# Kernel optimization log

Measured on AMD Instinct MI355X. Metric: run time of the kernel, lower is better.

Reference implementation:

```python
import jax, jax.numpy as jnp
import numpy as np

B, C, D, L, CTX = 8, 320, 24, 77, 768
NUM_GROUPS = 32
EPS = 1e-5


def setup_inputs() -> dict:
    key = jax.random.key(0)
    ks = jax.random.split(key, 8)
    s = 0.02
    return {
        "x": jax.random.normal(ks[0], (B, C, D, D, D), jnp.float32),
        "context": jax.random.normal(ks[1], (B, L, CTX), jnp.float32),
        "Wq": jax.random.normal(ks[2], (C, C), jnp.float32) * s,
        "bq": jnp.zeros((C,), jnp.float32),
        "Wk": jax.random.normal(ks[3], (C, CTX), jnp.float32) * s,
        "bk": jnp.zeros((C,), jnp.float32),
        "Wv": jax.random.normal(ks[4], (C, CTX), jnp.float32) * s,
        "bv": jnp.zeros((C,), jnp.float32),
        "Wo": jax.random.normal(ks[5], (C, C), jnp.float32) * s,
        "bo": jnp.zeros((C,), jnp.float32),
        "gamma": jnp.ones((C,), jnp.float32),
        "beta": jnp.zeros((C,), jnp.float32),
    }


def reference(x, context, Wq, bq, Wk, bk, Wv, bv, Wo, bo, gamma, beta):
    b, c = x.shape[:2]
    spatial = x.shape[2:]
    xf = x.reshape(b, c, -1)                                # [B, C, N]
    # 1x1 Conv3d == per-position channel matmul
    q = jnp.einsum('oc,bcn->bon', Wq, xf) + bq[None, :, None]
    ctx_t = context.transpose(0, 2, 1)                      # [B, CTX, L]
    k = jnp.einsum('oc,bcl->bol', Wk, ctx_t) + bk[None, :, None]
    v = jnp.einsum('oc,bcl->bol', Wv, ctx_t) + bv[None, :, None]
    # scores [B, N, L], scaled by C^-0.5 (int(C) in the original)
    qk = jnp.einsum('bcn,bcl->bnl', q, k) * (float(c) ** -0.5)
    w = jax.nn.softmax(qk, axis=-1)
    h = jnp.einsum('bcl,bnl->bcn', v, w)                    # [B, C, N]
    h = jnp.einsum('oc,bcn->bon', Wo, h) + bo[None, :, None]
    xr = h + xf                                             # residual
    # GroupNorm over (C/G, spatial) per group
    g = NUM_GROUPS
    xg = xr.reshape(b, g, -1)
    mu = jnp.mean(xg, axis=-1, keepdims=True)
    var = jnp.var(xg, axis=-1, keepdims=True)
    xn = ((xg - mu) * jax.lax.rsqrt(var + EPS)).reshape(b, c, -1)
    xn = xn * gamma[None, :, None] + beta[None, :, None]
    out = xn * jax.nn.sigmoid(xn)                           # Swish
    return out.reshape(b, c, *spatial)
```

## Files before the change

kernel.cpp:

```cpp
#include <hip/hip_runtime.h>
#include <hip/hip_bf16.h>

#define B_ 8
#define C_ 320
#define N_ 13824
#define L_ 77
#define LP 80
#define LV 96
#define CTXD 768
#define CPG 10
#define EPS_ 1e-5f
#define SCALE_ 0.05590169943749474f

typedef __attribute__((__ext_vector_type__(4))) float f32x4;
typedef __attribute__((__ext_vector_type__(8))) short s16x8;

#define WS_ACCUM 0
#define WS_T     2048
#define WS_KST   4608
#define WS_VST   414208
#define WS_K2F   823808
#define WS_V2F   1233408
#define WS_WQT   1724928
#define WS_WO    1929728
#define WS_WGF   2134528

__device__ __forceinline__ unsigned short f2bf(float f) {
  union { float f; unsigned u; } v; v.f = f;
  unsigned r = v.u + 0x7FFFu + ((v.u >> 16) & 1u);
  return (unsigned short)(r >> 16);
}
__device__ __forceinline__ float bf2f(unsigned short s) {
  union { unsigned u; float f; } v; v.u = ((unsigned)s) << 16;
  return v.f;
}
__device__ __forceinline__ s16x8 cvt8(const float* p) {
  f32x4 a = *reinterpret_cast<const f32x4*>(p);
  f32x4 b = *reinterpret_cast<const f32x4*>(p + 4);
  s16x8 r;
  r[0] = (short)f2bf(a[0]); r[1] = (short)f2bf(a[1]);
  r[2] = (short)f2bf(a[2]); r[3] = (short)f2bf(a[3]);
  r[4] = (short)f2bf(b[0]); r[5] = (short)f2bf(b[1]);
  r[6] = (short)f2bf(b[2]); r[7] = (short)f2bf(b[3]);
  return r;
}
__device__ __forceinline__ f32x4 MFMA(s16x8 a, s16x8 b, f32x4 c) {
  return __builtin_amdgcn_mfma_f32_16x16x32_bf16(a, b, c, 0, 0, 0);
}

__global__ __launch_bounds__(256) void prep_kernel(const float* __restrict__ Wq,
                                                   const float* __restrict__ Wo,
                                                   const float* __restrict__ ctx,
                                                   const float* __restrict__ Wk,
                                                   const float* __restrict__ bk,
                                                   const float* __restrict__ Wv,
                                                   const float* __restrict__ bv,
                                                   unsigned short* __restrict__ wqT,
                                                   unsigned short* __restrict__ wo_bf,
                                                   unsigned short* __restrict__ kst,
                                                   unsigned short* __restrict__ vst,
                                                   float* __restrict__ zws) {
  int bid = blockIdx.x;
  if (bid < 400) {
    int t = bid * 256 + threadIdx.x;
    if (t >= C_ * C_) return;
    int o = t / C_, c = t - o * C_;
    wqT[c * C_ + o] = f2bf(Wq[t]);
    wo_bf[t] = f2bf(Wo[t]);
    return;
  }
  int kb = bid - 400;
  { int t = kb * 256 + threadIdx.x; if (t < 1152) zws[t] = 0.f; }
  int lt = kb % 5;
  int kb5 = kb / 5;
  int b = kb5 / 5;
  int oc = kb5 % 5;
  int w = threadIdx.x >> 6, lane = threadIdx.x & 63;
  int r = lane & 15, h = lane >> 4;
  int o_row = oc * 64 + w * 16 + r;
  int l = lt * 16 + r;
  bool lok = (l < L_);
  f32x4 ak = {}, av = {};
  for (int ks = 0; ks < 24; ++ks) {
    int c0 = ks * 32 + h * 8;
    s16x8 aWk = cvt8(Wk + o_row * CTXD + c0);
    s16x8 aWv = cvt8(Wv + o_row * CTXD + c0);
    s16x8 bfr = {0,0,0,0,0,0,0,0};
    if (lok) bfr = cvt8(ctx + (b * L_ + l) * CTXD + c0);
    ak = MFMA(aWk, bfr, ak);
    av = MFMA(aWv, bfr, av);
  }
#pragma unroll
  for (int j = 0; j < 4; ++j) {
    int o = oc * 64 + w * 16 + h * 4 + j;
    float bkv = bk[o], bvv = bv[o];
    unsigned short kw = lok ? f2bf(SCALE_ * (ak[j] + bkv)) : (unsigned short)0;
    unsigned short vw = lok ? f2bf(av[j] + bvv) : (unsigned short)0;
    kst[(b * LP + l) * C_ + o] = kw;
    vst[(b * LP + l) * C_ + o] = vw;
  }
}

__global__ __launch_bounds__(256) void kv2_kernel(const unsigned short* __restrict__ wqT,
                                                  const unsigned short* __restrict__ wo_bf,
                                                  const unsigned short* __restrict__ kst,
                                                  const unsigned short* __restrict__ vst,
                                                  const float* __restrict__ bq,
                                                  float* __restrict__ tbuf,
                                                  unsigned short* __restrict__ k2F,
                                                  unsigned short* __restrict__ v2F) {
  int b = blockIdx.x / 5;
  int cc = blockIdx.x % 5;
  int w = threadIdx.x >> 6, lane = threadIdx.x & 63;
  int r = lane & 15, h = lane >> 4;
  int c_row = cc * 64 + w * 16 + r;
  f32x4 a2[5] = {}, av[5] = {};
#pragma unroll
  for (int ks = 0; ks < 10; ++ks) {
    int o0 = ks * 32 + h * 8;
    s16x8 aq = *reinterpret_cast<const s16x8*>(wqT + c_row * C_ + o0);
    s16x8 ao = *reinterpret_cast<const s16x8*>(wo_bf + c_row * C_ + o0);
#pragma unroll
    for (int nt = 0; nt < 5; ++nt) {
      int l = nt * 16 + r;
      s16x8 bk_ = *reinterpret_cast<const s16x8*>(kst + (b * LP + l) * C_ + o0);
      s16x8 bv_ = *reinterpret_cast<const s16x8*>(vst + (b * LP + l) * C_ + o0);
      a2[nt] = MFMA(aq, bk_, a2[nt]);
      av[nt] = MFMA(ao, bv_, av[nt]);
    }
  }
#pragma unroll
  for (int j = 0; j < 4; ++j) {
    int c = cc * 64 + w * 16 + h * 4 + j;
    int ks2 = c >> 5, h2 = (c >> 3) & 3, j2 = c & 7;
    int cs = c / 80, mt = (c - cs * 80) >> 4, rc = c & 15;
#pragma unroll
    for (int nt = 0; nt < 5; ++nt) {
      int l = nt * 16 + r;
      k2F[(((b * 5 + nt) * 10 + ks2) << 9) + ((h2 * 16 + r) << 3) + j2] = f2bf(a2[nt][j]);
      int ksl = l >> 5, hl = (l >> 3) & 3, jl = l & 7;
      v2F[((((long)(b * 4 + cs) * 5 + mt) * 3 + ksl) << 9) + ((hl * 16 + rc) << 3) + jl]
          = f2bf(av[nt][j]);
    }
  }
  {
    int t = threadIdx.x;
    int m = cc * 4 + (t >> 6);
    int cs = m / 5, mt = m % 5;
    long base = (((long)(b * 4 + cs) * 5 + mt) * 3 + 2) << 9;
    *reinterpret_cast<unsigned long long*>(v2F + base + 256 + (t & 63) * 4) = 0ull;
  }
  if (cc == 0 && threadIdx.x < LP) {
    int l = threadIdx.x;
    float acc = 0.f;
    for (int o8 = 0; o8 < C_; o8 += 8) {
      s16x8 kv = *reinterpret_cast<const s16x8*>(kst + (b * LP + l) * C_ + o8);
#pragma unroll
      for (int j = 0; j < 8; ++j) acc += bq[o8 + j] * bf2f((unsigned short)kv[j]);
    }
    tbuf[b * LP + l] = acc;
  }
}

__global__ __launch_bounds__(256)
__attribute__((amdgpu_waves_per_eu(2, 3)))
void fusedS_kernel(const float* __restrict__ x,
                   const unsigned short* __restrict__ k2F,
                   const float* __restrict__ tbuf,
                   unsigned short* __restrict__ wglF) {
  __shared__ __align__(16) unsigned short tile[64][344];
  char* tb = (char*)&tile[0][0];
  int bid = blockIdx.x;
  int b = bid & 7;
  int tileIdx = bid >> 3;
  int n0 = tileIdx * 64;
  int tid = threadIdx.x;
  int w = tid >> 6, lane = tid & 63, r = lane & 15, h = lane >> 4;
  const unsigned short* k2f = k2F + ((long)b * 50 << 9);

  s16x8 kfA[5], kfB[5];
#pragma unroll
  for (int nt = 0; nt < 5; ++nt)
    kfA[nt] = *reinterpret_cast<const s16x8*>(k2f + ((nt * 10) << 9) + (lane << 3));

  {
    int s_ = tid & 15;
    int cp = tid >> 4;
    const float* xb = x + (long)b * C_ * N_ + n0 + s_ * 4;
    f32x4 va[10], vb[10];
#pragma unroll
    for (int it = 0; it < 10; ++it) {
      const float* p = xb + (long)(it * 32 + cp * 2) * N_;
      va[it] = *reinterpret_cast<const f32x4*>(p);
      vb[it] = *reinterpret_cast<const f32x4*>(p + N_);
    }
#pragma unroll
    for (int it = 0; it < 10; ++it) {
      int cbyte = (it * 32 + cp * 2) * 2;
#pragma unroll
      for (int q = 0; q < 4; ++q) {
        int row = s_ * 4 + q;
        unsigned pk = (unsigned)f2bf(va[it][q]) | ((unsigned)f2bf(vb[it][q]) << 16);
        *reinterpret_cast<unsigned*>(tb + row * 688 + (cbyte ^ (row & 48))) = pk;
      }
    }
  }
  __syncthreads();

  int arow = w * 16 + r;
  int abase = arow * 688;
  int akey = arow & 48;
  f32x4 sacc[5] = {};
#define SCHUNK(KS, KC, KN)                                                      \
  {                                                                             \
    s16x8 a = *reinterpret_cast<const s16x8*>(                                  \
        tb + abase + (((KS * 32 + h * 8) * 2) ^ akey));                         \
    if (KS < 9) {                                                               \
      _Pragma("unroll") for (int nt = 0; nt < 5; ++nt)                          \
          KN[nt] = *reinterpret_cast<const s16x8*>(                             \
              k2f + ((nt * 10 + KS + 1) << 9) + (lane << 3));                   \
    }                                                                           \
    _Pragma("unroll") for (int nt = 0; nt < 5; ++nt)                            \
      sacc[nt] = MFMA(a, KC[nt], sacc[nt]);                                     \
  }
  SCHUNK(0, kfA, kfB) SCHUNK(1, kfB, kfA) SCHUNK(2, kfA, kfB)
  SCHUNK(3, kfB, kfA) SCHUNK(4, kfA, kfB) SCHUNK(5, kfB, kfA)
  SCHUNK(6, kfA, kfB) SCHUNK(7, kfB, kfA) SCHUNK(8, kfA, kfB)
  SCHUNK(9, kfB, kfA)
#undef SCHUNK

#pragma unroll
  for (int nt = 0; nt < 5; ++nt) {
    float tl = tbuf[b * LP + nt * 16 + r];
#pragma unroll
    for (int j = 0; j < 4; ++j) sacc[nt][j] += tl;
  }
  long wbase = ((long)(b * 216 + tileIdx) * 12) << 9;
  bool maskpad = (r >= 13);
#pragma unroll
  for (int j = 0; j < 4; ++j) {
    float m = -1e30f;
#pragma unroll
    for (int nt = 0; nt < 5; ++nt) {
      float v = (nt == 4 && maskpad) ? -1e30f : sacc[nt][j];
      m = fmaxf(m, v);
    }
    for (int d = 1; d < 16; d <<= 1) m = fmaxf(m, __shfl_xor(m, d));
    float e[5]; float sum = 0.f;
#pragma unroll
    for (int nt = 0; nt < 5; ++nt) {
      float v = (nt == 4 && maskpad) ? 0.f : __expf(sacc[nt][j] - m);
      e[nt] = v; sum += v;
    }
    for (int d = 1; d < 16; d <<= 1) sum += __shfl_xor(sum, d);
    float inv = 1.f / sum;
    int r2 = h * 4 + j;
#pragma unroll
    for (int nt = 0; nt < 5; ++nt) {
      int l = nt * 16 + r;
      int ks = l >> 5, h2 = (l >> 3) & 3, j2 = l & 7;
      wglF[wbase + ((ks * 4 + w) << 9) + ((h2 * 16 + r2) << 3) + j2] = f2bf(e[nt] * inv);
    }
  }
  {
    int t = tid;
    *reinterpret_cast<unsigned long long*>(
        wglF + wbase + ((2 * 4 + (t >> 6)) << 9) + 256 + (t & 63) * 4) = 0ull;
  }
}

__global__ __launch_bounds__(256)
__attribute__((amdgpu_waves_per_eu(2, 3)))
void mainH_kernel(const float* __restrict__ x,
                  const unsigned short* __restrict__ wglF,
                  const unsigned short* __restrict__ v2F,
                  const float* __restrict__ bo,
                  float* __restrict__ accum,
                  float* __restrict__ hout) {
  __shared__ float ch[C_][2];
  int bid = blockIdx.x;
  int b = bid & 7;
  int tileIdx = bid >> 3;
  int n0 = tileIdx * 64;
  int tid = threadIdx.x;
  int w = tid >> 6, lane = tid & 63, r = lane & 15, h = lane >> 4;
  const unsigned short* wf = wglF + (((long)(b * 216 + tileIdx) * 12) << 9);
  const unsigned short* vf = v2F + (((long)(b * 4 + w) * 15) << 9);
  const float* xb = x + (long)b * C_ * N_ + n0;

  f32x4 acc[4][5] = {};
#pragma unroll
  for (int ks = 0; ks < 3; ++ks) {
    s16x8 bf[4];
#pragma unroll
    for (int nt = 0; nt < 4; ++nt)
      bf[nt] = *reinterpret_cast<const s16x8*>(wf + ((ks * 4 + nt) << 9) + (lane << 3));
#pragma unroll
    for (int mt = 0; mt < 5; ++mt) {
      s16x8 va = *reinterpret_cast<const s16x8*>(vf + ((mt * 3 + ks) << 9) + (lane << 3));
#pragma unroll
      for (int nt = 0; nt < 4; ++nt) acc[nt][mt] = MFMA(va, bf[nt], acc[nt][mt]);
    }
  }
#pragma unroll
  for (int mt = 0; mt < 5; ++mt) {
    int cb = w * 80 + mt * 16 + h * 4;
    float bov[4];
#pragma unroll
    for (int j = 0; j < 4; ++j) bov[j] = bo[cb + j];
    float sv[4] = {0.f, 0.f, 0.f, 0.f}, sq[4] = {0.f, 0.f, 0.f, 0.f};
#pragma unroll
    for (int nt = 0; nt < 4; ++nt) {
      int n = nt * 16 + r;
#pragma unroll
      for (int j = 0; j < 4; ++j) {
        float val = acc[nt][mt][j] + bov[j] + xb[(long)(cb + j) * N_ + n];
        long e = ((long)b * C_ + cb + j) * N_ + n0 + n;
        *reinterpret_cast<unsigned short*>(
            (char*)hout + ((e >> 11) << 13) + ((e & 2047) << 1)) = f2bf(val);
        sv[j] += val; sq[j] += val * val;
      }
    }
#pragma unroll
    for (int j = 0; j < 4; ++j) {
      for (int d = 1; d < 16; d <<= 1) {
        sv[j] += __shfl_xor(sv[j], d);
        sq[j] += __shfl_xor(sq[j], d);
      }
      if (r == 0) { ch[cb + j][0] = sv[j]; ch[cb + j][1] = sq[j]; }
    }
  }
  __syncthreads();
  if (tid < 32) {
    float s0 = 0.f, s1 = 0.f;
#pragma unroll
    for (int i = 0; i < CPG; ++i) { s0 += ch[tid * CPG + i][0]; s1 += ch[tid * CPG + i][1]; }
    atomicAdd(&accum[b * 64 + tid * 2], s0);
    atomicAdd(&accum[b * 64 + tid * 2 + 1], s1);
  }
}

__global__ __launch_bounds__(256) void norm_kernel(float* __restrict__ hout,
                                                   const float* __restrict__ accum,
                                                   const float* __restrict__ gamma,
                                                   const float* __restrict__ beta) {
  long idx0 = (long)blockIdx.x * 2048;
  int t = threadIdx.x;
  s16x8 hv = *reinterpret_cast<const s16x8*>((const char*)hout + idx0 * 4 + t * 16);
  __syncthreads();
  long idx = idx0 + (long)t * 8;
  int b = (int)(idx / ((long)C_ * N_));
  long rem = idx - (long)b * C_ * N_;
  int c = (int)(rem / N_);
  int g = c / CPG;
  float s0 = accum[b * 64 + g * 2], s1 = accum[b * 64 + g * 2 + 1];
  const float invc = 1.f / 138240.f;
  float mu = s0 * invc;
  float var = s1 * invc - mu * mu;
  float rstd = rsqrtf(var + EPS_);
  float ga = gamma[c], be = beta[c];
  f32x4 v0, v1;
#pragma unroll
  for (int q = 0; q < 4; ++q) {
    float y = (bf2f((unsigned short)hv[q]) - mu) * rstd * ga + be;
    v0[q] = y / (1.f + __expf(-y));
    float z = (bf2f((unsigned short)hv[q + 4]) - mu) * rstd * ga + be;
    v1[q] = z / (1.f + __expf(-z));
  }
  __builtin_nontemporal_store(v0, reinterpret_cast<f32x4*>(hout + idx));
  __builtin_nontemporal_store(v1, reinterpret_cast<f32x4*>(hout + idx + 4));
}

extern "C" void kernel_launch(void* const* d_in, const int* in_sizes, int n_in,
                              void* d_out, int out_size, void* d_ws, size_t ws_size,
                              hipStream_t stream) {
  const float* x     = (const float*)d_in[0];
  const float* ctx   = (const float*)d_in[1];
  const float* Wq    = (const float*)d_in[2];
  const float* bq    = (const float*)d_in[3];
  const float* Wk    = (const float*)d_in[4];
  const float* bk    = (const float*)d_in[5];
  const float* Wv    = (const float*)d_in[6];
  const float* bv    = (const float*)d_in[7];
  const float* Wo    = (const float*)d_in[8];
  const float* bo    = (const float*)d_in[9];
  const float* gamma = (const float*)d_in[10];
  const float* beta  = (const float*)d_in[11];
  float* out = (float*)d_out;
  char* ws = (char*)d_ws;

  float* accum = (float*)(ws + WS_ACCUM);
  float* tbuf  = (float*)(ws + WS_T);
  unsigned short* kst  = (unsigned short*)(ws + WS_KST);
  unsigned short* vst  = (unsigned short*)(ws + WS_VST);
  unsigned short* k2F  = (unsigned short*)(ws + WS_K2F);
  unsigned short* v2F  = (unsigned short*)(ws + WS_V2F);
  unsigned short* wqT  = (unsigned short*)(ws + WS_WQT);
  unsigned short* wo_b = (unsigned short*)(ws + WS_WO);
  unsigned short* wglF = (unsigned short*)(ws + WS_WGF);

  prep_kernel<<<dim3(600), dim3(256), 0, stream>>>(Wq, Wo, ctx, Wk, bk, Wv, bv,
                                                   wqT, wo_b, kst, vst, (float*)ws);
  kv2_kernel<<<dim3(40), dim3(256), 0, stream>>>(wqT, wo_b, kst, vst, bq, tbuf, k2F, v2F);
  fusedS_kernel<<<dim3(1728), dim3(256), 0, stream>>>(x, k2F, tbuf, wglF);
  mainH_kernel<<<dim3(1728), dim3(256), 0, stream>>>(x, wglF, v2F, bo, accum, out);
  norm_kernel<<<dim3(17280), dim3(256), 0, stream>>>(out, accum, gamma, beta);
}
```

Baseline: 181.7 us.

## Fuse score-softmax and PV/output kernels, keep weights and residual in LDS

Merges the softmax-weights kernel and the V-projection/residual kernel into one. Attention weights stay in shared memory instead of being written to and read back from global memory. The residual now comes from the bf16 x tile already staged in LDS, so the second fp32 read of x is dropped. This cuts one launch and a large amount of global traffic. The cost is more LDS per block, which may lower occupancy, and a residual rounded to bf16.

New measurement: 169.5 us, median of 2. -6.7%, faster.

```diff
diff --git a/kernel.cpp b/kernel.cpp
--- a/kernel.cpp
+++ b/kernel.cpp
@@ -23,7 +23,6 @@
 #define WS_V2F   1233408
 #define WS_WQT   1724928
 #define WS_WO    1929728
-#define WS_WGF   2134528
 
 __device__ __forceinline__ unsigned short f2bf(float f) {
   union { float f; unsigned u; } v; v.f = f;
@@ -164,16 +163,20 @@
 
 __global__ __launch_bounds__(256)
 __attribute__((amdgpu_waves_per_eu(2, 3)))
-void fusedS_kernel(const float* __restrict__ x,
-                   const unsigned short* __restrict__ k2F,
-                   const float* __restrict__ tbuf,
-                   unsigned short* __restrict__ wglF) {
+void fused_kernel(const float* __restrict__ x,
+                  const unsigned short* __restrict__ k2F,
+                  const unsigned short* __restrict__ v2F,
+                  const float* __restrict__ tbuf,
+                  const float* __restrict__ bo,
+                  float* __restrict__ accum,
+                  float* __restrict__ hout) {
   __shared__ __align__(16) unsigned short tile[64][344];
+  __shared__ __align__(16) unsigned short pw[12][512];
+  __shared__ float ch[C_][2];
   char* tb = (char*)&tile[0][0];
   int bid = blockIdx.x;
   int b = bid & 7;
-  int tileIdx = bid >> 3;
-  int n0 = tileIdx * 64;
+  int n0 = (bid >> 3) * 64;
   int tid = threadIdx.x;
   int w = tid >> 6, lane = tid & 63, r = lane & 15, h = lane >> 4;
   const unsigned short* k2f = k2F + ((long)b * 50 << 9);
@@ -205,6 +208,7 @@
       }
     }
   }
+  *reinterpret_cast<unsigned long long*>(&pw[8 + (tid >> 6)][256 + (tid & 63) * 4]) = 0ull;
   __syncthreads();
 
   int arow = w * 16 + r;
@@ -235,7 +239,6 @@
 #pragma unroll
     for (int j = 0; j < 4; ++j) sacc[nt][j] += tl;
   }
-  long wbase = ((long)(b * 216 + tileIdx) * 12) << 9;
   bool maskpad = (r >= 13);
 #pragma unroll
   for (int j = 0; j < 4; ++j) {
@@ -259,42 +262,19 @@
     for (int nt = 0; nt < 5; ++nt) {
       int l = nt * 16 + r;
       int ks = l >> 5, h2 = (l >> 3) & 3, j2 = l & 7;
-      wglF[wbase + ((ks * 4 + w) << 9) + ((h2 * 16 + r2) << 3) + j2] = f2bf(e[nt] * inv);
-    }
-  }
-  {
-    int t = tid;
-    *reinterpret_cast<unsigned long long*>(
-        wglF + wbase + ((2 * 4 + (t >> 6)) << 9) + 256 + (t & 63) * 4) = 0ull;
-  }
-}
-
-__global__ __launch_bounds__(256)
-__attribute__((amdgpu_waves_per_eu(2, 3)))
-void mainH_kernel(const float* __restrict__ x,
-                  const unsigned short* __restrict__ wglF,
-                  const unsigned short* __restrict__ v2F,
-                  const float* __restrict__ bo,
-                  float* __restrict__ accum,
-                  float* __restrict__ hout) {
-  __shared__ float ch[C_][2];
-  int bid = blockIdx.x;
-  int b = bid & 7;
-  int tileIdx = bid >> 3;
-  int n0 = tileIdx * 64;
-  int tid = threadIdx.x;
-  int w = tid >> 6, lane = tid & 63, r = lane & 15, h = lane >> 4;
-  const unsigned short* wf = wglF + (((long)(b * 216 + tileIdx) * 12) << 9);
+      pw[ks * 4 + w][((h2 * 16 + r2) << 3) + j2] = f2bf(e[nt] * inv);
+    }
+  }
+  __syncthreads();
+
   const unsigned short* vf = v2F + (((long)(b * 4 + w) * 15) << 9);
-  const float* xb = x + (long)b * C_ * N_ + n0;
-
   f32x4 acc[4][5] = {};
 #pragma unroll
   for (int ks = 0; ks < 3; ++ks) {
     s16x8 bf[4];
 #pragma unroll
     for (int nt = 0; nt < 4; ++nt)
-      bf[nt] = *reinterpret_cast<const s16x8*>(wf + ((ks * 4 + nt) << 9) + (lane << 3));
+      bf[nt] = *reinterpret_cast<const s16x8*>(&pw[ks * 4 + nt][lane << 3]);
 #pragma unroll
     for (int mt = 0; mt < 5; ++mt) {
       s16x8 va = *reinterpret_cast<const s16x8*>(vf + ((mt * 3 + ks) << 9) + (lane << 3));
@@ -305,6 +285,7 @@
 #pragma unroll
   for (int mt = 0; mt < 5; ++mt) {
     int cb = w * 80 + mt * 16 + h * 4;
+    int cbyte = cb * 2;
     float bov[4];
 #pragma unroll
     for (int j = 0; j < 4; ++j) bov[j] = bo[cb + j];
@@ -312,9 +293,11 @@
 #pragma unroll
     for (int nt = 0; nt < 4; ++nt) {
       int n = nt * 16 + r;
+      unsigned long long xr4 = *reinterpret_cast<const unsigned long long*>(
+          tb + n * 688 + (cbyte ^ (n & 48)));
 #pragma unroll
       for (int j = 0; j < 4; ++j) {
-        float val = acc[nt][mt][j] + bov[j] + xb[(long)(cb + j) * N_ + n];
+        float val = acc[nt][mt][j] + bov[j] + bf2f((unsigned short)(xr4 >> (j * 16)));
         long e = ((long)b * C_ + cb + j) * N_ + n0 + n;
         *reinterpret_cast<unsigned short*>(
             (char*)hout + ((e >> 11) << 13) + ((e & 2047) << 1)) = f2bf(val);
@@ -397,12 +380,10 @@
   unsigned short* v2F  = (unsigned short*)(ws + WS_V2F);
   unsigned short* wqT  = (unsigned short*)(ws + WS_WQT);
   unsigned short* wo_b = (unsigned short*)(ws + WS_WO);
-  unsigned short* wglF = (unsigned short*)(ws + WS_WGF);
 
   prep_kernel<<<dim3(600), dim3(256), 0, stream>>>(Wq, Wo, ctx, Wk, bk, Wv, bv,
                                                    wqT, wo_b, kst, vst, (float*)ws);
   kv2_kernel<<<dim3(40), dim3(256), 0, stream>>>(wqT, wo_b, kst, vst, bq, tbuf, k2F, v2F);
-  fusedS_kernel<<<dim3(1728), dim3(256), 0, stream>>>(x, k2F, tbuf, wglF);
-  mainH_kernel<<<dim3(1728), dim3(256), 0, stream>>>(x, wglF, v2F, bo, accum, out);
+  fused_kernel<<<dim3(1728), dim3(256), 0, stream>>>(x, k2F, v2F, tbuf, bo, accum, out);
   norm_kernel<<<dim3(17280), dim3(256), 0, stream>>>(out, accum, gamma, beta);
 }
```
